# Performance work log

Measured on AMD Instinct MI355X. Metric: run time of the kernel, lower is better.

The kernel has to match this reference:

```python
import jax, jax.numpy as jnp
import numpy as np

B, T, C = 2, 2048, 1024
H = 16
DH = C // H  # 64
EPS = 1e-5


def setup_inputs() -> dict:
    key = jax.random.key(0)
    ks = jax.random.split(key, 12)
    s = lambda k, shape, fan: jax.random.normal(k, shape, jnp.float32) / np.sqrt(fan)
    return {
        'x': jax.random.normal(ks[0], (B, T, C), jnp.float32),
        'wq': s(ks[1], (H, C, DH), C),
        'wk': s(ks[2], (H, C, DH), C),
        'wv': s(ks[3], (H, C, DH), C),
        'w_proj': s(ks[4], (C, C), C),
        'b_proj': jnp.zeros((C,), jnp.float32),
        'g_ln1': jnp.ones((C,), jnp.float32),
        'b_ln1': jnp.zeros((C,), jnp.float32),
        'g_ln2': jnp.ones((C,), jnp.float32),
        'b_ln2': jnp.zeros((C,), jnp.float32),
        'w_ff1': s(ks[5], (C, 4 * C), C),
        'b_ff1': jnp.zeros((4 * C,), jnp.float32),
        'w_ff2': s(ks[6], (4 * C, C), 4 * C),
        'b_ff2': jnp.zeros((C,), jnp.float32),
    }


def _layernorm(x, g, b):
    mu = jnp.mean(x, axis=-1, keepdims=True)
    var = jnp.mean(jnp.square(x - mu), axis=-1, keepdims=True)
    return (x - mu) * jax.lax.rsqrt(var + EPS) * g + b


def _attention(x, wq, wk, wv, w_proj, b_proj):
    # per-head projections, batched over heads: [B,T,C] x [H,C,Dh] -> [B,H,T,Dh]
    q = jnp.einsum('btc,hcd->bhtd', x, wq)
    k = jnp.einsum('btc,hcd->bhtd', x, wk)
    v = jnp.einsum('btc,hcd->bhtd', x, wv)
    scores = jnp.einsum('bhtd,bhsd->bhts', q, k) / np.sqrt(DH).astype(np.float32)
    t = x.shape[1]
    causal = jnp.tril(jnp.ones((t, t), bool))
    scores = jnp.where(causal, scores, -jnp.inf)
    w = jax.nn.softmax(scores, axis=-1)
    out = jnp.einsum('bhts,bhsd->bhtd', w, v)  # [B,H,T,Dh]
    # concat heads (head order matches torch cat over head list)
    out = out.transpose(0, 2, 1, 3).reshape(x.shape[0], t, C)
    return out @ w_proj + b_proj


def reference(x, wq, wk, wv, w_proj, b_proj, g_ln1, b_ln1, g_ln2, b_ln2, w_ff1, b_ff1, w_ff2, b_ff2):
    x = x + _attention(_layernorm(x, g_ln1, b_ln1), wq, wk, wv, w_proj, b_proj)
    h = _layernorm(x, g_ln2, b_ln2)
    ff = jax.nn.relu(h @ w_ff1 + b_ff1) @ w_ff2 + b_ff2
    return x + ff
```

## Files before the change

kernel.cpp:

```cpp
#include <hip/hip_runtime.h>

#define DEV __device__ __forceinline__

typedef __attribute__((ext_vector_type(4))) float f32x4;
typedef __attribute__((ext_vector_type(8))) short short8;
typedef __attribute__((ext_vector_type(8))) __bf16 bf16x8;

DEV unsigned short f2bf(float f) {
  __bf16 h = (__bf16)f;
  return __builtin_bit_cast(unsigned short, h);
}
DEV unsigned pack2(float a, float b) {
  return (unsigned)f2bf(a) | ((unsigned)f2bf(b) << 16);
}
DEV bf16x8 ld_bf8(const unsigned short* p) {
  short8 v = *(const short8*)p;
  return __builtin_bit_cast(bf16x8, v);
}
DEV f32x4 MFMA(bf16x8 a, bf16x8 b, f32x4 c) {
  return __builtin_amdgcn_mfma_f32_16x16x32_bf16(a, b, c, 0, 0, 0);
}

typedef const __attribute__((address_space(1))) void GV;
typedef __attribute__((address_space(3))) void LV;
DEV void gl_lds16(const void* g, void* l) {
  __builtin_amdgcn_global_load_lds((GV*)g, (LV*)l, 16, 0, 0);
}

DEV void xcd_decode(int gx, int& bx, int& by) {
  const int nwg = gridDim.x, bid = blockIdx.x;
  const int cpx = nwg >> 3;
  const int swz = (bid & 7) * cpx + (bid >> 3);
  by = swz / gx;
  bx = swz % gx;
}

__global__ void __launch_bounds__(256) ln_fused(
    const float* __restrict__ x, const float* __restrict__ g,
    const float* __restrict__ b, unsigned short* __restrict__ y)
{
  const int row = blockIdx.x, tid = threadIdx.x;
  const float4 xv = ((const float4*)(x + (size_t)row * 1024))[tid];
  float s  = xv.x + xv.y + xv.z + xv.w;
  float s2 = xv.x * xv.x + xv.y * xv.y + xv.z * xv.z + xv.w * xv.w;
#pragma unroll
  for (int o = 32; o > 0; o >>= 1) { s += __shfl_down(s, o); s2 += __shfl_down(s2, o); }
  __shared__ float ps[4], ps2[4];
  if ((tid & 63) == 0) { ps[tid >> 6] = s; ps2[tid >> 6] = s2; }
  __syncthreads();
  float S  = ps[0] + ps[1] + ps[2] + ps[3];
  float S2 = ps2[0] + ps2[1] + ps2[2] + ps2[3];
  float mu = S * (1.f / 1024.f);
  float rs = rsqrtf(S2 * (1.f / 1024.f) - mu * mu + 1e-5f);
  const float4 gv = ((const float4*)g)[tid];
  const float4 bv = ((const float4*)b)[tid];
  uint2 r;
  r.x = pack2((xv.x - mu) * rs * gv.x + bv.x, (xv.y - mu) * rs * gv.y + bv.y);
  r.y = pack2((xv.z - mu) * rs * gv.z + bv.z, (xv.w - mu) * rs * gv.w + bv.w);
  ((uint2*)(y + (size_t)row * 1024))[tid] = r;
}

__global__ void __launch_bounds__(256) transp_f2b(
    const float* __restrict__ src, unsigned short* __restrict__ dst, int R, int C)
{
  __shared__ float t[64][65];
  const int c0 = blockIdx.x * 64, r0 = blockIdx.y * 64;
  const int tx = threadIdx.x & 63, tq = threadIdx.x >> 6;
#pragma unroll
  for (int i = 0; i < 16; i++) {
    int r = tq * 16 + i;
    t[r][tx] = src[(size_t)(r0 + r) * C + c0 + tx];
  }
  __syncthreads();
#pragma unroll
  for (int i = 0; i < 16; i++) {
    int c = tq * 16 + i;
    dst[(size_t)(c0 + c) * R + r0 + tx] = f2bf(t[tx][c]);
  }
}

__global__ void __launch_bounds__(256) qkv_transp(
    const float* __restrict__ wq, const float* __restrict__ wk,
    const float* __restrict__ wv, unsigned short* __restrict__ dst)
{
  __shared__ float t[64][65];
  const int c0 = blockIdx.x * 64, h = blockIdx.y, z = blockIdx.z;
  const float* w = (z == 0 ? wq : z == 1 ? wk : wv) + (size_t)h * 1024 * 64;
  const int tx = threadIdx.x & 63, tq = threadIdx.x >> 6;
#pragma unroll
  for (int i = 0; i < 16; i++) {
    int c = tq * 16 + i;
    t[c][tx] = w[(size_t)(c0 + c) * 64 + tx];
  }
  __syncthreads();
  unsigned short* drow = dst + (size_t)(z * 1024 + h * 64) * 1024 + c0;
#pragma unroll
  for (int i = 0; i < 16; i++) {
    int d = tq * 16 + i;
    drow[(size_t)d * 1024 + tx] = f2bf(t[tx][d]);
  }
}

__global__ void __launch_bounds__(256) v_transp(
    const unsigned short* __restrict__ qkv, unsigned short* __restrict__ vt)
{
  __shared__ unsigned s[64][65];
  const int t0 = blockIdx.x * 64, h = blockIdx.y, b = blockIdx.z;
  const int tx = threadIdx.x & 63, tq = threadIdx.x >> 6;
#pragma unroll
  for (int i = 0; i < 16; i++) {
    int tr = tq * 16 + i;
    s[tr][tx] = qkv[(size_t)(b * 2048 + t0 + tr) * 3072 + 2048 + h * 64 + tx];
  }
  __syncthreads();
  unsigned short* vb = vt + (size_t)((b * 16 + h) * 64) * 2048 + t0;
#pragma unroll
  for (int i = 0; i < 16; i++) {
    int d = tq * 16 + i;
    vb[(size_t)d * 2048 + tx] = (unsigned short)s[tx][d];
  }
}

template<int BIAS, int RELU, int RES, int OBF>
__global__ void __launch_bounds__(256) gemm_bt(
    const unsigned short* __restrict__ A, const unsigned short* __restrict__ Bt,
    const float* __restrict__ bias, const float* __restrict__ res,
    void* __restrict__ out, int M, int N, int K, int gx)
{
  __shared__ unsigned short As[2][128 * 32];
  __shared__ unsigned short Bs[2][128 * 32];
  int bx, by;
  xcd_decode(gx, bx, by);
  const int tid = threadIdx.x;
  const int wid = tid >> 6, lane = tid & 63;
  const int lg = lane >> 4, lr = lane & 15;
  const int m0 = by * 128, n0 = bx * 128;
  const int wr = (wid >> 1) * 64, wc = (wid & 1) * 64;

  const int srow = tid >> 2;
  const int scs = (tid & 3) ^ (srow & 3);
  const unsigned short* ga = A + (size_t)(m0 + srow) * K + scs * 8;
  const unsigned short* gb = Bt + (size_t)(n0 + srow) * K + scs * 8;
  const int ca = (lg ^ (lr & 3)) * 8;

  f32x4 acc[4][4] = {};

  auto stage = [&](int buf, int k0) {
    char* asb = (char*)&As[buf][0] + wid * 1024;
    char* bsb = (char*)&Bs[buf][0] + wid * 1024;
    gl_lds16(ga + k0, asb);
    gl_lds16(ga + k0 + (size_t)64 * K, asb + 4096);
    gl_lds16(gb + k0, bsb);
    gl_lds16(gb + k0 + (size_t)64 * K, bsb + 4096);
  };

  stage(0, 0);
  int cur = 0;
  for (int k0 = 0; k0 < K; k0 += 32) {
    __syncthreads();
    if (k0 + 32 < K) stage(cur ^ 1, k0 + 32);
    bf16x8 a[4], b[4];
#pragma unroll
    for (int m = 0; m < 4; m++) a[m] = ld_bf8(&As[cur][(wr + m * 16 + lr) * 32 + ca]);
#pragma unroll
    for (int n = 0; n < 4; n++) b[n] = ld_bf8(&Bs[cur][(wc + n * 16 + lr) * 32 + ca]);
#pragma unroll
    for (int m = 0; m < 4; m++)
#pragma unroll
      for (int n = 0; n < 4; n++)
        acc[m][n] = MFMA(a[m], b[n], acc[m][n]);
    cur ^= 1;
  }

#pragma unroll
  for (int m = 0; m < 4; m++) {
    const int row0 = m0 + wr + m * 16 + lg * 4;
#pragma unroll
    for (int n = 0; n < 4; n++) {
      const int col = n0 + wc + n * 16 + lr;
      const float bv = BIAS ? bias[col] : 0.f;
#pragma unroll
      for (int r = 0; r < 4; r++) {
        const size_t off = (size_t)(row0 + r) * N + col;
        float v = acc[m][n][r] + bv;
        if (RES) v += res[off];
        if (RELU) v = v > 0.f ? v : 0.f;
        if (OBF) ((unsigned short*)out)[off] = f2bf(v);
        else     ((float*)out)[off] = v;
      }
    }
  }
}

template<int BIAS, int RELU, int RES, int OBF>
__global__ void __launch_bounds__(256) gemm_64(
    const unsigned short* __restrict__ A, const unsigned short* __restrict__ Bt,
    const float* __restrict__ bias, const float* __restrict__ res,
    void* __restrict__ out, int M, int N, int K, int gx)
{
  __shared__ unsigned short As[2][64 * 64];
  __shared__ unsigned short Bs[2][64 * 64];
  int bx, by;
  xcd_decode(gx, bx, by);
  const int tid = threadIdx.x;
  const int wid = tid >> 6, lane = tid & 63;
  const int lg = lane >> 4, lr = lane & 15;
  const int m0 = by * 64, n0 = bx * 64;
  const int wr = (wid >> 1) * 32, wc = (wid & 1) * 32;

  const int srow = tid >> 3;
  const int scs = (tid & 7) ^ (srow & 7);
  const unsigned short* ga = A + (size_t)(m0 + srow) * K + scs * 8;
  const unsigned short* gb = Bt + (size_t)(n0 + srow) * K + scs * 8;
  const int lxs = lr & 7;

  f32x4 acc[2][2] = {};

  auto stage = [&](int buf, int k0) {
    char* asb = (char*)&As[buf][0] + wid * 1024;
    char* bsb = (char*)&Bs[buf][0] + wid * 1024;
    gl_lds16(ga + k0, asb);
    gl_lds16(ga + k0 + (size_t)32 * K, asb + 4096);
    gl_lds16(gb + k0, bsb);
    gl_lds16(gb + k0 + (size_t)32 * K, bsb + 4096);
  };

  stage(0, 0);
  int cur = 0;
  for (int k0 = 0; k0 < K; k0 += 64) {
    __syncthreads();
    if (k0 + 64 < K) stage(cur ^ 1, k0 + 64);
#pragma unroll
    for (int kk = 0; kk < 2; kk++) {
      const int cb = kk * 4;
      bf16x8 a[2], b[2];
#pragma unroll
      for (int m = 0; m < 2; m++)
        a[m] = ld_bf8(&As[cur][(wr + m * 16 + lr) * 64 + ((cb + lg) ^ lxs) * 8]);
#pragma unroll
      for (int n = 0; n < 2; n++)
        b[n] = ld_bf8(&Bs[cur][(wc + n * 16 + lr) * 64 + ((cb + lg) ^ lxs) * 8]);
#pragma unroll
      for (int m = 0; m < 2; m++)
#pragma unroll
        for (int n = 0; n < 2; n++)
          acc[m][n] = MFMA(a[m], b[n], acc[m][n]);
    }
    cur ^= 1;
  }

#pragma unroll
  for (int m = 0; m < 2; m++) {
    const int row0 = m0 + wr + m * 16 + lg * 4;
#pragma unroll
    for (int n = 0; n < 2; n++) {
      const int col = n0 + wc + n * 16 + lr;
      const float bv = BIAS ? bias[col] : 0.f;
#pragma unroll
      for (int r = 0; r < 4; r++) {
        const size_t off = (size_t)(row0 + r) * N + col;
        float v = acc[m][n][r] + bv;
        if (RES) v += res[off];
        if (RELU) v = v > 0.f ? v : 0.f;
        if (OBF) ((unsigned short*)out)[off] = f2bf(v);
        else     ((float*)out)[off] = v;
      }
    }
  }
}

__global__ void __launch_bounds__(256) attn_fwd(
    const unsigned short* __restrict__ qkv, const unsigned short* __restrict__ vt,
    unsigned short* __restrict__ out)
{
  __shared__ unsigned short Ks[2][64 * 64];
  __shared__ unsigned short Vs[2][64 * 64];
  __shared__ unsigned short P[4][16][72];

  const int bid = blockIdx.x;
  const int swz = (bid & 7) * 128 + (bid >> 3);
  const int bh = swz >> 5;
  const int qt = 31 - (swz & 31);
  const int b = bh >> 4, h = bh & 15;
  const int tid = threadIdx.x, wid = tid >> 6, lane = tid & 63;
  const int lg = lane >> 4, lr = lane & 15;

  const int nkt = qt + 1;
  const float C2 = 0.18033688f;
  const float THRRAW = 44.3614f;

  const unsigned short* kbase = qkv + (size_t)(b * 2048) * 3072 + 1024 + h * 64;
  const unsigned short* vbase = vt + (size_t)(bh * 64) * 2048;

  const int sr = tid >> 3;
  const int sc = tid & 7;
  const int c0 = sc ^ (sr & 7);

  auto stage = [&](int buf, int kt) {
    const int kv0 = kt * 64;
    char* kd = (char*)&Ks[buf][0] + wid * 1024;
    char* vd = (char*)&Vs[buf][0] + wid * 1024;
    gl_lds16(kbase + (size_t)(kv0 + sr) * 3072 + c0 * 8, kd);
    gl_lds16(kbase + (size_t)(kv0 + 32 + sr) * 3072 + c0 * 8, kd + 4096);
    gl_lds16(vbase + (size_t)sr * 2048 + kv0 + c0 * 8, vd);
    gl_lds16(vbase + (size_t)(32 + sr) * 2048 + kv0 + c0 * 8, vd + 4096);
  };

  const unsigned short* qb = qkv + (size_t)(b * 2048) * 3072 + h * 64;
  const int qg = qt * 64 + wid * 16 + lr;
  const bf16x8 qf0 = ld_bf8(qb + (size_t)qg * 3072 + lg * 8);
  const bf16x8 qf1 = ld_bf8(qb + (size_t)qg * 3072 + 32 + lg * 8);

  f32x4 o[4] = {};
  float m = -1e30f, l = 0.f;

  stage(0, 0);
  __syncthreads();
  for (int kt = 0; kt < nkt; kt++) {
    const int buf = kt & 1;
    if (kt + 1 < nkt) stage(buf ^ 1, kt + 1);

    const int kv0 = kt * 64;
    const unsigned short* Kb = &Ks[buf][0];
    const unsigned short* Vb = &Vs[buf][0];
    f32x4 s[4] = {};
    __builtin_amdgcn_s_setprio(1);
#pragma unroll
    for (int f = 0; f < 4; f++) {
      const int row = f * 16 + lr;
      const int rc = row & 7;
      s[f] = MFMA(ld_bf8(Kb + row * 64 + (lg ^ rc) * 8), qf0, s[f]);
      s[f] = MFMA(ld_bf8(Kb + row * 64 + ((lg | 4) ^ rc) * 8), qf1, s[f]);
    }
    __builtin_amdgcn_s_setprio(0);
    float p[16];
    float mt = -1e30f;
    const bool diag = (kt == qt);
#pragma unroll
    for (int f = 0; f < 4; f++)
#pragma unroll
      for (int r = 0; r < 4; r++) {
        float sv = s[f][r];
        if (diag) {
          const int kv = kv0 + f * 16 + lg * 4 + r;
          sv = (kv <= qg) ? sv : -1e30f;
        }
        p[f * 4 + r] = sv;
        mt = fmaxf(mt, sv);
      }
    mt = fmaxf(mt, __shfl_xor(mt, 16));
    mt = fmaxf(mt, __shfl_xor(mt, 32));
    if (!__all(mt - m <= THRRAW)) {
      const float mnew = fmaxf(m, mt);
      const float sf = exp2f(C2 * (m - mnew));
      l *= sf;
#pragma unroll
      for (int df = 0; df < 4; df++) o[df] *= sf;
      m = mnew;
    }
    const float cm = C2 * m;
    float ps = 0.f;
#pragma unroll
    for (int i = 0; i < 16; i++) {
      p[i] = exp2f(fmaf(p[i], C2, -cm));
      ps += p[i];
    }
    ps += __shfl_xor(ps, 16);
    ps += __shfl_xor(ps, 32);
    l += ps;
    unsigned short* Pr = &P[wid][lr][0];
#pragma unroll
    for (int f = 0; f < 4; f++) {
      *(unsigned*)(Pr + f * 16 + lg * 4)     = pack2(p[f * 4 + 0], p[f * 4 + 1]);
      *(unsigned*)(Pr + f * 16 + lg * 4 + 2) = pack2(p[f * 4 + 2], p[f * 4 + 3]);
    }
    const bf16x8 pf0 = ld_bf8(Pr + lg * 8);
    const bf16x8 pf1 = ld_bf8(Pr + 32 + lg * 8);
    __builtin_amdgcn_s_setprio(1);
#pragma unroll
    for (int df = 0; df < 4; df++) {
      const int row = df * 16 + lr;
      const int rc = row & 7;
      o[df] = MFMA(ld_bf8(Vb + row * 64 + (lg ^ rc) * 8), pf0, o[df]);
      o[df] = MFMA(ld_bf8(Vb + row * 64 + ((lg | 4) ^ rc) * 8), pf1, o[df]);
    }
    __builtin_amdgcn_s_setprio(0);
    __syncthreads();
  }

  const float inv = 1.f / l;
  unsigned* orow = (unsigned*)(out + (size_t)(b * 2048 + qg) * 1024 + h * 64 + lg * 4);
#pragma unroll
  for (int df = 0; df < 4; df++) {
    orow[df * 8 + 0] = pack2(o[df][0] * inv, o[df][1] * inv);
    orow[df * 8 + 1] = pack2(o[df][2] * inv, o[df][3] * inv);
  }
}

extern "C" void kernel_launch(void* const* d_in, const int* in_sizes, int n_in,
                              void* d_out, int out_size, void* d_ws, size_t ws_size,
                              hipStream_t stream)
{
  const float* x     = (const float*)d_in[0];
  const float* wq    = (const float*)d_in[1];
  const float* wk    = (const float*)d_in[2];
  const float* wv    = (const float*)d_in[3];
  const float* wproj = (const float*)d_in[4];
  const float* bproj = (const float*)d_in[5];
  const float* gln1  = (const float*)d_in[6];
  const float* bln1  = (const float*)d_in[7];
  const float* gln2  = (const float*)d_in[8];
  const float* bln2  = (const float*)d_in[9];
  const float* wff1  = (const float*)d_in[10];
  const float* bff1  = (const float*)d_in[11];
  const float* wff2  = (const float*)d_in[12];
  const float* bff2  = (const float*)d_in[13];

  char* ws = (char*)d_ws;
  const size_t MB = 1u << 20;
  float*          x2    = (float*)         (ws + 0 * MB);
  unsigned short* hbuf  = (unsigned short*)(ws + 16 * MB);
  unsigned short* xn1   = (unsigned short*)(ws + 24 * MB);
  unsigned short* attn  = (unsigned short*)(ws + 24 * MB);
  unsigned short* qkvb  = (unsigned short*)(ws + 32 * MB);
  unsigned short* vtb   = (unsigned short*)(ws + 56 * MB);
  unsigned short* a1    = (unsigned short*)(ws + 32 * MB);
  unsigned short* wqkvT = (unsigned short*)(ws + 64 * MB);
  unsigned short* wprojT= (unsigned short*)(ws + 70 * MB);
  unsigned short* wff1T = (unsigned short*)(ws + 72 * MB);
  unsigned short* wff2T = (unsigned short*)(ws + 80 * MB);

  qkv_transp<<<dim3(16, 16, 3), 256, 0, stream>>>(wq, wk, wv, wqkvT);
  transp_f2b<<<dim3(16, 16), 256, 0, stream>>>(wproj, wprojT, 1024, 1024);
  transp_f2b<<<dim3(64, 16), 256, 0, stream>>>(wff1, wff1T, 1024, 4096);
  transp_f2b<<<dim3(16, 64), 256, 0, stream>>>(wff2, wff2T, 4096, 1024);

  ln_fused<<<4096, 256, 0, stream>>>(x, gln1, bln1, xn1);
  gemm_bt<0, 0, 0, 1><<<768, 256, 0, stream>>>(
      xn1, wqkvT, nullptr, nullptr, qkvb, 4096, 3072, 1024, 24);
  v_transp<<<dim3(32, 16, 2), 256, 0, stream>>>(qkvb, vtb);
  attn_fwd<<<1024, 256, 0, stream>>>(qkvb, vtb, attn);
  gemm_64<1, 0, 1, 0><<<1024, 256, 0, stream>>>(
      attn, wprojT, bproj, x, x2, 4096, 1024, 1024, 16);
  ln_fused<<<4096, 256, 0, stream>>>(x2, gln2, bln2, hbuf);
  gemm_bt<1, 1, 0, 1><<<1024, 256, 0, stream>>>(
      hbuf, wff1T, bff1, nullptr, a1, 4096, 4096, 1024, 32);
  gemm_64<1, 0, 1, 0><<<1024, 256, 0, stream>>>(
      a1, wff2T, bff2, x2, (float*)d_out, 4096, 1024, 4096, 16);
}
```

Before: 259.9 us.

## Double query tile per attention block to reuse staged K/V tiles

Each attention block now handles 128 query rows, with every wave owning two 16-row query slices, so each staged K/V tile feeds twice as many query rows and the grid halves to 512 blocks. The block-to-(batch,head,qtile) mapping is rewritten so each XCD gets a fixed set of 4 heads, with heavy and light causal tiles interleaved by a half/rank scheme. Tiles fully above the diagonal for a slice are skipped per slice. The cost is fewer blocks (less parallelism and load balance on a 256-CU part) and more registers per wave for the two accumulator sets.

```diff
diff --git a/kernel.cpp b/kernel.cpp
--- a/kernel.cpp
+++ b/kernel.cpp
@@ -278,14 +278,16 @@
   __shared__ unsigned short P[4][16][72];
 
   const int bid = blockIdx.x;
-  const int swz = (bid & 7) * 128 + (bid >> 3);
-  const int bh = swz >> 5;
-  const int qt = 31 - (swz & 31);
+  const int xcd = bid & 7, local = bid >> 3;
+  const int bh_l = local & 3;
+  const int half = local >> 5, rk = (local >> 2) & 7;
+  const int qt = half ? rk : 15 - rk;
+  const int bh = xcd * 4 + bh_l;
   const int b = bh >> 4, h = bh & 15;
   const int tid = threadIdx.x, wid = tid >> 6, lane = tid & 63;
   const int lg = lane >> 4, lr = lane & 15;
 
-  const int nkt = qt + 1;
+  const int nkt = (qt + 1) * 2;
   const float C2 = 0.18033688f;
   const float THRRAW = 44.3614f;
 
@@ -307,20 +309,20 @@
   };
 
   const unsigned short* qb = qkv + (size_t)(b * 2048) * 3072 + h * 64;
-  const int qg = qt * 64 + wid * 16 + lr;
-  const bf16x8 qf0 = ld_bf8(qb + (size_t)qg * 3072 + lg * 8);
-  const bf16x8 qf1 = ld_bf8(qb + (size_t)qg * 3072 + 32 + lg * 8);
-
-  f32x4 o[4] = {};
-  float m = -1e30f, l = 0.f;
-
-  stage(0, 0);
-  __syncthreads();
-  for (int kt = 0; kt < nkt; kt++) {
-    const int buf = kt & 1;
-    if (kt + 1 < nkt) stage(buf ^ 1, kt + 1);
-
+  const int qbase0 = qt * 128 + wid * 32;
+  const int qg0 = qbase0 + lr, qg1 = qbase0 + 16 + lr;
+  const bf16x8 q00 = ld_bf8(qb + (size_t)qg0 * 3072 + lg * 8);
+  const bf16x8 q01 = ld_bf8(qb + (size_t)qg0 * 3072 + 32 + lg * 8);
+  const bf16x8 q10 = ld_bf8(qb + (size_t)qg1 * 3072 + lg * 8);
+  const bf16x8 q11 = ld_bf8(qb + (size_t)qg1 * 3072 + 32 + lg * 8);
+
+  f32x4 o0[4] = {}, o1[4] = {};
+  float m0 = -1e30f, l0 = 0.f, m1 = -1e30f, l1 = 0.f;
+
+  auto proc = [&](int kt, int qgbase, int qg, const bf16x8& qf0, const bf16x8& qf1,
+                  f32x4 (&o)[4], float& m, float& l, int buf) {
     const int kv0 = kt * 64;
+    if (kv0 > qgbase + 15) return;
     const unsigned short* Kb = &Ks[buf][0];
     const unsigned short* Vb = &Vs[buf][0];
     f32x4 s[4] = {};
@@ -335,7 +337,7 @@
     __builtin_amdgcn_s_setprio(0);
     float p[16];
     float mt = -1e30f;
-    const bool diag = (kt == qt);
+    const bool diag = (kv0 + 63 > qgbase);
 #pragma unroll
     for (int f = 0; f < 4; f++)
 #pragma unroll
@@ -385,15 +387,35 @@
       o[df] = MFMA(ld_bf8(Vb + row * 64 + ((lg | 4) ^ rc) * 8), pf1, o[df]);
     }
     __builtin_amdgcn_s_setprio(0);
+  };
+
+  stage(0, 0);
+  __syncthreads();
+  for (int kt = 0; kt < nkt; kt++) {
+    const int buf = kt & 1;
+    if (kt + 1 < nkt) stage(buf ^ 1, kt + 1);
+    proc(kt, qbase0, qg0, q00, q01, o0, m0, l0, buf);
+    proc(kt, qbase0 + 16, qg1, q10, q11, o1, m1, l1, buf);
     __syncthreads();
   }
 
-  const float inv = 1.f / l;
-  unsigned* orow = (unsigned*)(out + (size_t)(b * 2048 + qg) * 1024 + h * 64 + lg * 4);
-#pragma unroll
-  for (int df = 0; df < 4; df++) {
-    orow[df * 8 + 0] = pack2(o[df][0] * inv, o[df][1] * inv);
-    orow[df * 8 + 1] = pack2(o[df][2] * inv, o[df][3] * inv);
+  {
+    const float inv = 1.f / l0;
+    unsigned* orow = (unsigned*)(out + (size_t)(b * 2048 + qg0) * 1024 + h * 64 + lg * 4);
+#pragma unroll
+    for (int df = 0; df < 4; df++) {
+      orow[df * 8 + 0] = pack2(o0[df][0] * inv, o0[df][1] * inv);
+      orow[df * 8 + 1] = pack2(o0[df][2] * inv, o0[df][3] * inv);
+    }
+  }
+  {
+    const float inv = 1.f / l1;
+    unsigned* orow = (unsigned*)(out + (size_t)(b * 2048 + qg1) * 1024 + h * 64 + lg * 4);
+#pragma unroll
+    for (int df = 0; df < 4; df++) {
+      orow[df * 8 + 0] = pack2(o1[df][0] * inv, o1[df][1] * inv);
+      orow[df * 8 + 1] = pack2(o1[df][2] * inv, o1[df][3] * inv);
+    }
   }
 }
 
@@ -439,7 +461,7 @@
   gemm_bt<0, 0, 0, 1><<<768, 256, 0, stream>>>(
       xn1, wqkvT, nullptr, nullptr, qkvb, 4096, 3072, 1024, 24);
   v_transp<<<dim3(32, 16, 2), 256, 0, stream>>>(qkvb, vtb);
-  attn_fwd<<<1024, 256, 0, stream>>>(qkvb, vtb, attn);
+  attn_fwd<<<512, 256, 0, stream>>>(qkvb, vtb, attn);
   gemm_64<1, 0, 1, 0><<<1024, 256, 0, stream>>>(
       attn, wprojT, bproj, x, x2, 4096, 1024, 1024, 16);
   ln_fused<<<4096, 256, 0, stream>>>(x2, gln2, bln2, hbuf);
```

Result: slower. 272.5 us (+4.8%).
